# Kernel optimization log

Measured on AMD Instinct MI355X. Metric: run time of the kernel, lower is better.

The kernel has to match this reference:

```python
import jax, jax.numpy as jnp
import numpy as np

N, E, D, H, LAYERS = 50000, 800000, 128, 8, 2
LRELU_ALPHA = 0.2


def _seg_softmax(logits, seg, n):
    # numerically stable softmax over edges grouped by destination node
    m = jax.ops.segment_max(logits, seg, num_segments=n)
    z = jnp.exp(logits - m[seg])
    s = jax.ops.segment_sum(z, seg, num_segments=n)
    return z / jnp.maximum(s[seg], 1e-16)


def _gat_layer(x, src, dst, W, a_src, a_dst, concat):
    # W: [H, Fin, F'], a_src/a_dst: [H, F']
    n = x.shape[0]
    outs = []
    for h in range(W.shape[0]):  # loop over heads to bound peak memory
        Wh = x @ W[h]                              # [N, F']
        es = Wh @ a_src[h]                         # [N]
        ed = Wh @ a_dst[h]                         # [N]
        e = jax.nn.leaky_relu(es[src] + ed[dst], LRELU_ALPHA)  # [E]
        att = _seg_softmax(e, dst, n)              # [E]
        out = jax.ops.segment_sum(att[:, None] * Wh[src], dst, num_segments=n)
        outs.append(out)
    if concat:
        return jax.nn.elu(jnp.concatenate(outs, axis=-1))  # [N, H*F']
    return jnp.mean(jnp.stack(outs, axis=0), axis=0)        # [N, F']


def _rel_gcn_layer(x, src, dst, w, W):
    # weighted-adjacency GCN with row (in-degree) normalization + ReLU
    n = x.shape[0]
    deg = jax.ops.segment_sum(w, dst, num_segments=n)
    norm = w / jnp.maximum(deg[dst], 1e-16)        # [E]
    h = x @ W                                      # [N, Dout]
    agg = jax.ops.segment_sum(norm[:, None] * h[src], dst, num_segments=n)
    return jax.nn.relu(agg)


def setup_inputs() -> dict:
    key = jax.random.key(0)
    ks = jax.random.split(key, 12)
    s = 1.0 / np.sqrt(D)
    return {
        "x": jax.random.normal(ks[0], (N, D), dtype=jnp.float32),
        "edge_index": jax.random.randint(ks[1], (2, E), 0, N, dtype=jnp.int64),
        "edge_weight": jax.random.uniform(ks[2], (E,), dtype=jnp.float32),
        "gat_W0": jax.random.normal(ks[3], (H, D, D // H), dtype=jnp.float32) * s,
        "gat_a0_src": jax.random.normal(ks[4], (H, D // H), dtype=jnp.float32) * s,
        "gat_a0_dst": jax.random.normal(ks[5], (H, D // H), dtype=jnp.float32) * s,
        "gat_W1": jax.random.normal(ks[6], (H, D, D), dtype=jnp.float32) * s,
        "gat_a1_src": jax.random.normal(ks[7], (H, D), dtype=jnp.float32) * s,
        "gat_a1_dst": jax.random.normal(ks[8], (H, D), dtype=jnp.float32) * s,
        "gcn_W0": jax.random.normal(ks[9], (D, D), dtype=jnp.float32) * s,
        "gcn_W1": jax.random.normal(ks[10], (D, D), dtype=jnp.float32) * s,
    }


def reference(x, edge_index, edge_weight, gat_W0, gat_a0_src, gat_a0_dst,
              gat_W1, gat_a1_src, gat_a1_dst, gcn_W0, gcn_W1):
    src, dst = edge_index[0], edge_index[1]
    gat_params = [(gat_W0, gat_a0_src, gat_a0_dst), (gat_W1, gat_a1_src, gat_a1_dst)]
    gcn_params = [gcn_W0, gcn_W1]
    x1, x2 = x, x  # dropout is identity in eval mode
    for i in range(LAYERS):
        W, a_s, a_d = gat_params[i]
        x1 = _gat_layer(x1, src, dst, W, a_s, a_d, concat=(i != LAYERS - 1))
        x2 = _rel_gcn_layer(x2, src, dst, edge_weight, gcn_params[i])
    # cat along new last dim then MaxPool1d(2) == elementwise max of branches
    return jnp.maximum(x1, x2)
```

## Files before the change

### kernel.cpp

```cpp
#include <hip/hip_runtime.h>

#define LRELU_ALPHA 0.2f

typedef __attribute__((ext_vector_type(8))) short short8;
typedef __attribute__((ext_vector_type(4))) float float4v;
typedef __attribute__((ext_vector_type(2))) float f32x2;

__device__ __forceinline__ unsigned short f2bf(float f) {
  union { float f; unsigned u; } x; x.f = f;
  unsigned r = (x.u + 0x7fff + ((x.u >> 16) & 1)) >> 16;
  return (unsigned short)r;
}
__device__ __forceinline__ float bflo(unsigned u) {
  union { unsigned u; float f; } x; x.u = u << 16; return x.f;
}
__device__ __forceinline__ float bfhi(unsigned u) {
  union { unsigned u; float f; } x; x.u = u & 0xffff0000u; return x.f;
}
__device__ __forceinline__ f32x2 bfpair(unsigned u) {
  return (f32x2){bflo(u), bfhi(u)};
}
__device__ __forceinline__ unsigned packbf(float a, float b) {
  return (unsigned)f2bf(a) | ((unsigned)f2bf(b) << 16);
}


__global__ __launch_bounds__(256) void k_count(const int* __restrict__ dst,
                                               int* __restrict__ cnt, int E) {
  int e = blockIdx.x * 256 + threadIdx.x;
  if (e < E) atomicAdd(&cnt[dst[e]], 1);
}

__global__ __launch_bounds__(1024) void k_scan1(const int* __restrict__ cnt,
                                                int* __restrict__ lscan,
                                                int* __restrict__ bsum, int N) {
  __shared__ int sm[1024];
  int t = threadIdx.x;
  int base = blockIdx.x * 1024;
  int v = (base + t < N) ? cnt[base + t] : 0;
  sm[t] = v;
  __syncthreads();
  for (int off = 1; off < 1024; off <<= 1) {
    int x = (t >= off) ? sm[t - off] : 0;
    __syncthreads();
    sm[t] += x;
    __syncthreads();
  }
  if (base + t < N) lscan[base + t] = sm[t] - v;
  if (t == 1023) bsum[blockIdx.x] = sm[1023];
}

__global__ __launch_bounds__(64) void k_scan2(int* __restrict__ bsum,
                                              int* __restrict__ rowptrN, int nb) {
  int t = threadIdx.x;
  int v = (t < nb) ? bsum[t] : 0;
  int orig = v;
  for (int off = 1; off < 64; off <<= 1) {
    int y = __shfl_up(v, off, 64);
    if (t >= off) v += y;
  }
  if (t < nb) bsum[t] = v - orig;
  if (t == 63) *rowptrN = v;
}

__global__ __launch_bounds__(1024) void k_scan3(int* __restrict__ rowptr,
                                                int* __restrict__ cur,
                                                const int* __restrict__ bsum, int N) {
  int i = blockIdx.x * 1024 + threadIdx.x;
  if (i < N) {
    int v = rowptr[i] + bsum[blockIdx.x];
    rowptr[i] = v;
    cur[i] = v;
  }
}

__global__ __launch_bounds__(256) void k_scatter(const int* __restrict__ src,
                                                 const int* __restrict__ dst,
                                                 const float* __restrict__ w,
                                                 const float* __restrict__ logit0,
                                                 int* __restrict__ cur,
                                                 uint2* __restrict__ edata,
                                                 unsigned short* __restrict__ pedge,
                                                 int E) {
  int base = (blockIdx.x * 256 + threadIdx.x) * 4;
  if (base >= E) return;
  int n = E - base; if (n > 4) n = 4;
  int ss[4], dd[4]; float ww[4];
  if (n == 4) {
    int4 s4 = *(const int4*)(src + base);
    int4 d4 = *(const int4*)(dst + base);
    float4 w4 = *(const float4*)(w + base);
    ss[0] = s4.x; ss[1] = s4.y; ss[2] = s4.z; ss[3] = s4.w;
    dd[0] = d4.x; dd[1] = d4.y; dd[2] = d4.z; dd[3] = d4.w;
    ww[0] = w4.x; ww[1] = w4.y; ww[2] = w4.z; ww[3] = w4.w;
  } else {
    for (int i = 0; i < n; ++i) { ss[i] = src[base + i]; dd[i] = dst[base + i]; ww[i] = w[base + i]; }
  }
  int pp[4];
#pragma unroll
  for (int i = 0; i < 4; ++i)
    if (i < n) pp[i] = atomicAdd(&cur[dd[i]], 1);
#pragma unroll
  for (int i = 0; i < 4; ++i) {
    if (i >= n) break;
    int s = ss[i], d = dd[i], p = pp[i];
    edata[p] = make_uint2((unsigned)s, __float_as_uint(ww[i]));
    float4 es0 = *(const float4*)(logit0 + (size_t)s * 16);
    float4 es1 = *(const float4*)(logit0 + (size_t)s * 16 + 4);
    float4 ed0 = *(const float4*)(logit0 + (size_t)d * 16 + 8);
    float4 ed1 = *(const float4*)(logit0 + (size_t)d * 16 + 12);
    float lg[8] = {es0.x + ed0.x, es0.y + ed0.y, es0.z + ed0.z, es0.w + ed0.w,
                   es1.x + ed1.x, es1.y + ed1.y, es1.z + ed1.z, es1.w + ed1.w};
    unsigned short o[8];
#pragma unroll
    for (int h = 0; h < 8; ++h) {
      float v = lg[h] > 0.f ? lg[h] : LRELU_ALPHA * lg[h];
      o[h] = f2bf(__expf(fminf(v, 80.f)));
    }
    ushort4 q0 = {o[0], o[1], o[2], o[3]};
    ushort4 q1 = {o[4], o[5], o[6], o[7]};
    *(ushort4*)(pedge + (size_t)p * 8) = q0;
    *(ushort4*)(pedge + (size_t)p * 8 + 4) = q1;
  }
}

__global__ __launch_bounds__(256) void k_pack(const float* __restrict__ W0,
                                              const float* __restrict__ a0s,
                                              const float* __restrict__ a0d,
                                              const float* __restrict__ W1,
                                              const float* __restrict__ a1s,
                                              const float* __restrict__ a1d,
                                              const float* __restrict__ gw0,
                                              const float* __restrict__ gw1,
                                              unsigned short* __restrict__ W0catT,
                                              float* __restrict__ logitW,
                                              unsigned short* __restrict__ gw1T,
                                              unsigned short* __restrict__ va1T,
                                              unsigned short* __restrict__ WstackT) {
  int idx = blockIdx.x * 256 + threadIdx.x;
  if (idx < 32768) {
    int n = idx >> 7, k = idx & 127;
    float v;
    if (n < 128) {
      int h = n >> 4, f = n & 15;
      v = W0[h * 2048 + k * 16 + f];
    } else {
      v = gw0[k * 128 + (n - 128)];
    }
    W0catT[idx] = f2bf(v);
  } else if (idx < 34816) {
    int j = idx - 32768;
    int k = j >> 4, c = j & 15;
    int h = (c < 8) ? c : c - 8;
    const float* a = (c < 8) ? a0s : a0d;
    float s = 0.f;
    for (int f = 0; f < 16; ++f) s += W0[h * 2048 + k * 16 + f] * a[h * 16 + f];
    logitW[j] = s;
  } else if (idx < 51200) {
    int j = idx - 34816;
    int n = j >> 7, k = j & 127;
    gw1T[j] = f2bf(gw1[k * 128 + n]);
  } else if (idx < 53248) {
    int j = idx - 51200;
    int c = j >> 7, k = j & 127;
    int h = c & 7;
    const float* a = (c < 8) ? a1s : a1d;
    float s = 0.f;
    for (int f = 0; f < 128; ++f) s += W1[h * 16384 + k * 128 + f] * a[h * 128 + f];
    va1T[j] = f2bf(s);
  } else if (idx < 184320) {
    int j = idx - 53248;
    int n = j >> 10, kk = j & 1023;
    int h = kk >> 7, k = kk & 127;
    WstackT[j] = f2bf(W1[h * 16384 + k * 128 + n] * 0.125f);
  }
}

__global__ __launch_bounds__(256) void k_prep(const float* __restrict__ x,
                                              const float* __restrict__ logitW,
                                              unsigned short* __restrict__ xb,
                                              float* __restrict__ logit0, int N) {
  __shared__ float sm[16][132];
  __shared__ float sw[2048];
  int t = threadIdx.x;
  int base = blockIdx.x * 16;
  int r = t >> 4, cc = (t & 15) * 8;
  const float* xr = x + (size_t)(base + r) * 128 + cc;
  float4 v0 = *(const float4*)xr;
  float4 v1 = *(const float4*)(xr + 4);
  ushort4 o0 = {f2bf(v0.x), f2bf(v0.y), f2bf(v0.z), f2bf(v0.w)};
  ushort4 o1 = {f2bf(v1.x), f2bf(v1.y), f2bf(v1.z), f2bf(v1.w)};
  *(ushort4*)(xb + (size_t)(base + r) * 128 + cc) = o0;
  *(ushort4*)(xb + (size_t)(base + r) * 128 + cc + 4) = o1;
  *(float4*)&sm[r][cc] = v0;
  *(float4*)&sm[r][cc + 4] = v1;
  *(float4*)&sw[t * 8] = *(const float4*)(logitW + t * 8);
  *(float4*)&sw[t * 8 + 4] = *(const float4*)(logitW + t * 8 + 4);
  __syncthreads();
  int c = t & 15;
  float acc = 0.f;
#pragma unroll
  for (int k = 0; k < 128; ++k) acc += sm[r][k] * sw[k * 16 + c];
  logit0[(size_t)(base + r) * 16 + c] = acc;
}

__global__ __launch_bounds__(256) void k_pedge(const float* __restrict__ logits,
                                               const uint2* __restrict__ edata,
                                               const int* __restrict__ rowptr,
                                               unsigned short* __restrict__ pedge,
                                               float* __restrict__ linv, int N) {
  int wave = threadIdx.x >> 6, lane = threadIdx.x & 63;
  int d = blockIdx.x * 4 + wave;
  if (d >= N) return;
  int j8 = lane >> 3, h = lane & 7;
  float edv = logits[(size_t)d * 16 + 8 + h];
  int beg = rowptr[d], end = rowptr[d + 1];
  float lsum = 0.f;
  for (int ii = beg + j8; ii < end; ii += 8) {
    unsigned s = edata[ii].x;
    float es = logits[(size_t)s * 16 + h];
    float lg = es + edv;
    lg = lg > 0.f ? lg : LRELU_ALPHA * lg;
    float p = __expf(fminf(lg, 80.f));
    lsum += p;
    pedge[(size_t)ii * 8 + h] = f2bf(p);
  }
  lsum += __shfl_xor(lsum, 8, 64);
  lsum += __shfl_xor(lsum, 16, 64);
  lsum += __shfl_xor(lsum, 32, 64);
  if (lane < 8) linv[(size_t)d * 8 + h] = lsum > 0.f ? 1.f / lsum : 0.f;
}

template <int NT, int OUT_BF16, int EPI>
__global__ __launch_bounds__(256) void k_mgemm(const unsigned short* __restrict__ A, int lda,
                                               const unsigned short* __restrict__ BT, int ldb,
                                               void* __restrict__ Cv, int ldc,
                                               const void* __restrict__ aux,
                                               int M, int Ncols, int K) {
  __shared__ unsigned short As[64][64];
  __shared__ unsigned short Bs[NT * 16][64];
  int tid = threadIdx.x;
  int w = tid >> 6, lane = tid & 63;
  int quad = lane >> 4, l16 = lane & 15;
  int row0 = blockIdx.x * 64;
  int c0 = blockIdx.y * (NT * 16);
  float4v acc[NT];
#pragma unroll
  for (int t = 0; t < NT; ++t) acc[t] = (float4v){0.f, 0.f, 0.f, 0.f};

  for (int k0 = 0; k0 < K; k0 += 64) {
    __syncthreads();
#pragma unroll
    for (int i = 0; i < 2; ++i) {
      int c = tid + i * 256;
      int r = c >> 3, kc = c & 7;
      uint4 v = {0u, 0u, 0u, 0u};
      int gr = row0 + r;
      if (gr < M) v = *(const uint4*)(A + (size_t)gr * lda + k0 + kc * 8);
      *(uint4*)(&As[r][(kc ^ (r & 7)) * 8]) = v;
    }
#pragma unroll
    for (int i = 0; i < (NT * 128 + 255) / 256; ++i) {
      int c = tid + i * 256;
      if (c < NT * 128) {
        int n = c >> 3, kc = c & 7;
        uint4 v = {0u, 0u, 0u, 0u};
        int gn = c0 + n;
        if (gn < Ncols) v = *(const uint4*)(BT + (size_t)gn * ldb + k0 + kc * 8);
        *(uint4*)(&Bs[n][(kc ^ (n & 7)) * 8]) = v;
      }
    }
    __syncthreads();
#pragma unroll
    for (int ks = 0; ks < 2; ++ks) {
      int m = w * 16 + l16;
      int ga = (ks * 4 + quad) ^ (m & 7);
      short8 a = *(const short8*)(&As[m][ga * 8]);
#pragma unroll
      for (int t = 0; t < NT; ++t) {
        int n = t * 16 + l16;
        int gb = (ks * 4 + quad) ^ (n & 7);
        short8 b = *(const short8*)(&Bs[n][gb * 8]);
        acc[t] = __builtin_amdgcn_mfma_f32_16x16x32_bf16(a, b, acc[t], 0, 0, 0);
      }
    }
  }
#pragma unroll
  for (int t = 0; t < NT; ++t) {
    int cc = c0 + t * 16 + l16;
    if (cc >= Ncols) continue;
#pragma unroll
    for (int i = 0; i < 4; ++i) {
      int rr = row0 + w * 16 + quad * 4 + i;
      if (rr >= M) continue;
      float v = acc[t][i];
      if (EPI == 1) {
        unsigned short us = ((const unsigned short*)aux)[(size_t)rr * ldc + cc];
        v = fmaxf(v, bflo((unsigned)us));
      }
      if (EPI == 2) {
        ((unsigned short*)Cv)[(size_t)rr * 256 + 4 * (cc >> 1) + 2 + (cc & 1)] = f2bf(v);
      } else if (EPI == 4) {
        if (cc < 128) {
          ((unsigned short*)Cv)[(size_t)rr * 128 + cc] = f2bf(v);
        } else {
          int enc = __builtin_amdgcn_cvt_pk_fp8_f32(v, v, 0, false);
          ((unsigned char*)aux)[(size_t)rr * 128 + (cc - 128)] = (unsigned char)(enc & 0xff);
        }
      } else if (OUT_BF16)
        ((unsigned short*)Cv)[(size_t)rr * ldc + cc] = f2bf(v);
      else
        ((float*)Cv)[(size_t)rr * ldc + cc] = v;
    }
  }
}

__global__ __launch_bounds__(256) void k_agg0(const unsigned short* __restrict__ featg,
                                              const unsigned char* __restrict__ featc,
                                              const int* __restrict__ rowptr,
                                              const uint2* __restrict__ edata,
                                              const unsigned short* __restrict__ pedge,
                                              unsigned short* __restrict__ x1c,
                                              unsigned short* __restrict__ x2,
                                              unsigned short* __restrict__ xh, int N) {
  __shared__ uint2 swl[4][64];
  __shared__ float pl[4][512];
  int wave = threadIdx.x >> 6, lane = threadIdx.x & 63;
  int d = blockIdx.x * 4 + wave;
  if (d >= N) return;
  int half = lane >> 5, lane2 = lane & 31;
  int head = lane2 >> 2;
  int beg = rowptr[d], end = rowptr[d + 1], deg = end - beg;
  f32x2 aa = {0.f, 0.f}, ab = {0.f, 0.f}, ga = {0.f, 0.f}, gb = {0.f, 0.f};
  float l = 0.f, wsum = 0.f;
  for (int base = 0; base < deg; base += 64) {
    int idx = beg + base + lane;
    uint2 sv = make_uint2(0u, 0u);
    uint4 q = make_uint4(0u, 0u, 0u, 0u);
    if (idx < end) {
      sv = edata[idx];
      q = *(const uint4*)(pedge + (size_t)idx * 8);
    }
    swl[wave][lane] = sv;
    float4 pa = make_float4(bflo(q.x), bfhi(q.x), bflo(q.y), bfhi(q.y));
    float4 pb = make_float4(bflo(q.z), bfhi(q.z), bflo(q.w), bfhi(q.w));
    *(float4*)&pl[wave][lane * 8] = pa;
    *(float4*)&pl[wave][lane * 8 + 4] = pb;
    int ng = deg - base; if (ng > 64) ng = 64;
    int tp = (ng + 1) >> 1;
    int t = 0;
    for (; t + 2 <= tp; t += 2) {
      int e0 = 2 * t + half, e1 = e0 + 2;
      uint2 sw0 = swl[wave][e0], sw1 = swl[wave][e1];
      float p0 = pl[wave][e0 * 8 + head], p1 = pl[wave][e1 * 8 + head];
      uint2 g0 = ((const uint2*)featg)[(size_t)sw0.x * 32 + lane2];
      unsigned c0v = ((const unsigned*)featc)[(size_t)sw0.x * 32 + lane2];
      uint2 g1 = ((const uint2*)featg)[(size_t)sw1.x * 32 + lane2];
      unsigned c1v = ((const unsigned*)featc)[(size_t)sw1.x * 32 + lane2];
      float w0 = __uint_as_float(sw0.y), w1 = __uint_as_float(sw1.y);
      aa += bfpair(g0.x) * p0;
      ab += bfpair(g0.y) * p0;
      ga += __builtin_amdgcn_cvt_pk_f32_fp8(c0v, false) * w0;
      gb += __builtin_amdgcn_cvt_pk_f32_fp8(c0v, true) * w0;
      l += p0; wsum += w0;
      aa += bfpair(g1.x) * p1;
      ab += bfpair(g1.y) * p1;
      ga += __builtin_amdgcn_cvt_pk_f32_fp8(c1v, false) * w1;
      gb += __builtin_amdgcn_cvt_pk_f32_fp8(c1v, true) * w1;
      l += p1; wsum += w1;
    }
    for (; t < tp; ++t) {
      int e = 2 * t + half;
      uint2 sw = swl[wave][e];
      float p = pl[wave][e * 8 + head];
      float wj = __uint_as_float(sw.y);
      uint2 g = ((const uint2*)featg)[(size_t)sw.x * 32 + lane2];
      unsigned cv = ((const unsigned*)featc)[(size_t)sw.x * 32 + lane2];
      aa += bfpair(g.x) * p;
      ab += bfpair(g.y) * p;
      ga += __builtin_amdgcn_cvt_pk_f32_fp8(cv, false) * wj;
      gb += __builtin_amdgcn_cvt_pk_f32_fp8(cv, true) * wj;
      l += p; wsum += wj;
    }
  }
  aa.x += __shfl_xor(aa.x, 32, 64); aa.y += __shfl_xor(aa.y, 32, 64);
  ab.x += __shfl_xor(ab.x, 32, 64); ab.y += __shfl_xor(ab.y, 32, 64);
  ga.x += __shfl_xor(ga.x, 32, 64); ga.y += __shfl_xor(ga.y, 32, 64);
  gb.x += __shfl_xor(gb.x, 32, 64); gb.y += __shfl_xor(gb.y, 32, 64);
  l += __shfl_xor(l, 32, 64);
  wsum += __shfl_xor(wsum, 32, 64);
  if (half == 0) {
    float inv = l > 0.f ? 1.f / l : 0.f;
    float v0 = aa.x * inv, v1 = aa.y * inv, v2 = ab.x * inv, v3 = ab.y * inv;
    v0 = v0 > 0.f ? v0 : __expf(v0) - 1.f;
    v1 = v1 > 0.f ? v1 : __expf(v1) - 1.f;
    v2 = v2 > 0.f ? v2 : __expf(v2) - 1.f;
    v3 = v3 > 0.f ? v3 : __expf(v3) - 1.f;
    unsigned p0 = packbf(v0, v1), p1 = packbf(v2, v3);
    ((uint2*)x1c)[(size_t)d * 32 + lane2] = make_uint2(p0, p1);
    ((unsigned*)xh)[(size_t)d * 128 + 4 * lane2] = p0;
    ((unsigned*)xh)[(size_t)d * 128 + 4 * lane2 + 2] = p1;
    float ginv = 1.f / fmaxf(wsum, 1e-16f);
    float w0 = fmaxf(ga.x * ginv, 0.f), w1 = fmaxf(ga.y * ginv, 0.f);
    float w2 = fmaxf(gb.x * ginv, 0.f), w3 = fmaxf(gb.y * ginv, 0.f);
    ((uint2*)x2)[(size_t)d * 32 + lane2] = make_uint2(packbf(w0, w1), packbf(w2, w3));
  }
}

__global__ __launch_bounds__(256) void k_agg1(const unsigned short* __restrict__ xh,
                                              const int* __restrict__ rowptr,
                                              const uint2* __restrict__ edata,
                                              const unsigned short* __restrict__ pedge,
                                              const float* __restrict__ linv,
                                              unsigned short* __restrict__ aggbuf,
                                              unsigned short* __restrict__ x2f, int N) {
  __shared__ uint2 swl[4][64];
  __shared__ float pl[4][512];
  int wave = threadIdx.x >> 6, lane = threadIdx.x & 63;
  int d = blockIdx.x * 4 + wave;
  if (d >= N) return;
  int half = lane >> 5, lane2 = lane & 31;
  int beg = rowptr[d], end = rowptr[d + 1], deg = end - beg;
  f32x2 axA[8] = {}, axB[8] = {};
  f32x2 ga = {0.f, 0.f}, gb = {0.f, 0.f};
  float wsum = 0.f;
  for (int base = 0; base < deg; base += 64) {
    int idx = beg + base + lane;
    uint2 sv = make_uint2(0u, 0u);
    uint4 q = make_uint4(0u, 0u, 0u, 0u);
    if (idx < end) {
      sv = edata[idx];
      q = *(const uint4*)(pedge + (size_t)idx * 8);
    }
    swl[wave][lane] = sv;
    float4 pa = make_float4(bflo(q.x), bfhi(q.x), bflo(q.y), bfhi(q.y));
    float4 pb = make_float4(bflo(q.z), bfhi(q.z), bflo(q.w), bfhi(q.w));
    *(float4*)&pl[wave][lane * 8] = pa;
    *(float4*)&pl[wave][lane * 8 + 4] = pb;
    int ng = deg - base; if (ng > 64) ng = 64;
    int tp = (ng + 1) >> 1;
    for (int t = 0; t < tp; ++t) {
      int e = 2 * t + half;
      uint2 sw = swl[wave][e];
      float4 pv0 = *(const float4*)&pl[wave][e * 8];
      float4 pv1 = *(const float4*)&pl[wave][e * 8 + 4];
      float wj = __uint_as_float(sw.y);
      uint4 u = *(const uint4*)(xh + (size_t)sw.x * 256 + 8 * lane2);
      f32x2 xA = bfpair(u.x), hA = bfpair(u.y);
      f32x2 xB = bfpair(u.z), hB = bfpair(u.w);
      ga += hA * wj;
      gb += hB * wj;
      wsum += wj;
      axA[0] += xA * pv0.x; axB[0] += xB * pv0.x;
      axA[1] += xA * pv0.y; axB[1] += xB * pv0.y;
      axA[2] += xA * pv0.z; axB[2] += xB * pv0.z;
      axA[3] += xA * pv0.w; axB[3] += xB * pv0.w;
      axA[4] += xA * pv1.x; axB[4] += xB * pv1.x;
      axA[5] += xA * pv1.y; axB[5] += xB * pv1.y;
      axA[6] += xA * pv1.z; axB[6] += xB * pv1.z;
      axA[7] += xA * pv1.w; axB[7] += xB * pv1.w;
    }
  }
#pragma unroll
  for (int h = 0; h < 8; ++h) {
    axA[h].x += __shfl_xor(axA[h].x, 32, 64); axA[h].y += __shfl_xor(axA[h].y, 32, 64);
    axB[h].x += __shfl_xor(axB[h].x, 32, 64); axB[h].y += __shfl_xor(axB[h].y, 32, 64);
  }
  ga.x += __shfl_xor(ga.x, 32, 64); ga.y += __shfl_xor(ga.y, 32, 64);
  gb.x += __shfl_xor(gb.x, 32, 64); gb.y += __shfl_xor(gb.y, 32, 64);
  wsum += __shfl_xor(wsum, 32, 64);
  if (half == 0) {
    float4 i0 = *(const float4*)(linv + (size_t)d * 8);
    float4 i1 = *(const float4*)(linv + (size_t)d * 8 + 4);
    float invh[8] = {i0.x, i0.y, i0.z, i0.w, i1.x, i1.y, i1.z, i1.w};
    size_t lr2 = (size_t)d * 256;
#pragma unroll
    for (int h = 0; h < 8; ++h) {
      ((uint2*)aggbuf)[lr2 + h * 32 + lane2] =
          make_uint2(packbf(axA[h].x * invh[h], axA[h].y * invh[h]),
                     packbf(axB[h].x * invh[h], axB[h].y * invh[h]));
    }
    float ginv = 1.f / fmaxf(wsum, 1e-16f);
    float w0 = fmaxf(ga.x * ginv, 0.f), w1 = fmaxf(ga.y * ginv, 0.f);
    float w2 = fmaxf(gb.x * ginv, 0.f), w3 = fmaxf(gb.y * ginv, 0.f);
    ((uint2*)x2f)[(size_t)d * 32 + lane2] = make_uint2(packbf(w0, w1), packbf(w2, w3));
  }
}


extern "C" void kernel_launch(void* const* d_in, const int* in_sizes, int n_in,
                              void* d_out, int out_size, void* d_ws, size_t ws_size,
                              hipStream_t stream) {
  const float* x   = (const float*)d_in[0];
  const int*   ei  = (const int*)d_in[1];
  const float* ew  = (const float*)d_in[2];
  const float* W0  = (const float*)d_in[3];
  const float* a0s = (const float*)d_in[4];
  const float* a0d = (const float*)d_in[5];
  const float* W1  = (const float*)d_in[6];
  const float* a1s = (const float*)d_in[7];
  const float* a1d = (const float*)d_in[8];
  const float* gw0 = (const float*)d_in[9];
  const float* gw1 = (const float*)d_in[10];
  float* out = (float*)d_out;

  const int N = in_sizes[0] / 128;
  const int E = in_sizes[1] / 2;
  const int* src = ei;
  const int* dst = ei + E;

  char* p = (char*)d_ws;
  auto carve = [&](size_t bytes) {
    void* r = (void*)p;
    p += (bytes + 255) & ~(size_t)255;
    return r;
  };
  int*   cnt    = (int*)carve((size_t)N * 4);
  int*   rowptr = (int*)carve((size_t)(N + 1) * 4);
  int*   cur    = (int*)carve((size_t)N * 4);
  int*   bsum   = (int*)carve(256 * 4);
  uint2* edata  = (uint2*)carve((size_t)E * 8);
  unsigned short* W0catT  = (unsigned short*)carve(32768 * 2);
  float*          logitW  = (float*)carve(2048 * 4);
  unsigned short* gw1T    = (unsigned short*)carve(16384 * 2);
  unsigned short* va1T    = (unsigned short*)carve(2048 * 2);
  unsigned short* WstackT = (unsigned short*)carve(131072 * 2);
  unsigned short* x2   = (unsigned short*)carve((size_t)N * 128 * 2);
  float*          esed = (float*)carve((size_t)N * 16 * 4);
  unsigned short* xh   = (unsigned short*)carve((size_t)N * 256 * 2);
  unsigned short* pedge = (unsigned short*)carve((size_t)E * 8 * 2);
  float*          linv1 = (float*)carve((size_t)N * 8 * 4);
  size_t ph1 = ((size_t)N * 128 * 2 + 255) & ~(size_t)255;
  size_t ph2 = ph1 + (((size_t)N * 128 * 2 + 255) & ~(size_t)255);
  size_t ph3 = ph2 + (((size_t)N * 128 + 255) & ~(size_t)255);
  size_t ph4 = ph3 + (((size_t)N * 16 * 4 + 255) & ~(size_t)255);
  size_t scratch_sz = (size_t)N * 1024 * 2;
  if (ph4 > scratch_sz) scratch_sz = ph4;
  char* scratch = (char*)carve(scratch_sz);
  unsigned short* xb     = (unsigned short*)scratch;
  unsigned short* x1c    = (unsigned short*)scratch;
  unsigned short* featg  = (unsigned short*)(scratch + ph1);
  unsigned char*  featc  = (unsigned char*)(scratch + ph2);
  float*          logit0 = (float*)(scratch + ph3);
  unsigned short* aggbuf = (unsigned short*)scratch;
  unsigned short* x2f    = x2;

  int gE = (E + 255) / 256;
  int gE4 = ((E + 3) / 4 + 255) / 256;
  int nb = (N + 1023) / 1024;
  int gM = (N + 63) / 64;
  int gD = (N + 3) / 4;

  hipMemsetAsync(cnt, 0, (size_t)N * 4, stream);
  k_count<<<gE, 256, 0, stream>>>(dst, cnt, E);
  k_scan1<<<nb, 1024, 0, stream>>>(cnt, rowptr, bsum, N);
  k_scan2<<<1, 64, 0, stream>>>(bsum, rowptr + N, nb);
  k_scan3<<<nb, 1024, 0, stream>>>(rowptr, cur, bsum, N);

  k_pack<<<(184320 + 255) / 256, 256, 0, stream>>>(W0, a0s, a0d, W1, a1s, a1d, gw0,
                                                   gw1, W0catT, logitW, gw1T, va1T,
                                                   WstackT);
  k_prep<<<(N + 15) / 16, 256, 0, stream>>>(x, logitW, xb, logit0, N);

  k_scatter<<<gE4, 256, 0, stream>>>(src, dst, ew, logit0, cur, edata, pedge, E);

  k_mgemm<8, 1, 4><<<dim3(gM, 2), 256, 0, stream>>>(xb, 128, W0catT, 128, featg, 128,
                                                    featc, N, 256, 128);
  k_agg0<<<gD, 256, 0, stream>>>(featg, featc, rowptr, edata, pedge, x1c, x2, xh, N);

  k_mgemm<1, 0, 0><<<dim3(gM, 1), 256, 0, stream>>>(x1c, 128, va1T, 128, esed, 16,
                                                    nullptr, N, 16, 128);
  k_mgemm<8, 1, 2><<<dim3(gM, 1), 256, 0, stream>>>(x2, 128, gw1T, 128, xh, 256,
                                                    nullptr, N, 128, 128);

  k_pedge<<<gD, 256, 0, stream>>>(esed, edata, rowptr, pedge, linv1, N);

  k_agg1<<<gD, 256, 0, stream>>>(xh, rowptr, edata, pedge, linv1, aggbuf, x2f, N);

  k_mgemm<8, 0, 1><<<dim3(gM, 1), 256, 0, stream>>>(aggbuf, 1024, WstackT, 1024, out,
                                                    128, x2f, N, 128, 1024);
}
```

Measured before the change: 448.4 us.

## Use full-wave per-edge gathers and persistent grid-stride loops in aggregation kernels

The two edge-aggregation kernels now use all 64 lanes of a wave on one edge's feature row with narrower per-lane loads, instead of splitting the wave into two halves that handle alternate edges and then combining them with cross-lane shuffles. Each wave processes edges in groups of four to keep more independent gathers in flight. The grid is capped at 2048 blocks and each wave loops over destination nodes, with launch bounds raised to request 8 blocks per CU. This removes the shuffle reduction and halves per-lane register accumulators, but each load is narrower and low-degree nodes may leave fewer loads outstanding per wave.

Measured after the change: 458.6 us. 2.3% more time.

```diff
diff --git a/kernel.cpp b/kernel.cpp
--- a/kernel.cpp
+++ b/kernel.cpp
@@ -315,175 +315,164 @@
   }
 }
 
-__global__ __launch_bounds__(256) void k_agg0(const unsigned short* __restrict__ featg,
-                                              const unsigned char* __restrict__ featc,
-                                              const int* __restrict__ rowptr,
-                                              const uint2* __restrict__ edata,
-                                              const unsigned short* __restrict__ pedge,
-                                              unsigned short* __restrict__ x1c,
-                                              unsigned short* __restrict__ x2,
-                                              unsigned short* __restrict__ xh, int N) {
+__global__ __launch_bounds__(256, 8) void k_agg0(const unsigned short* __restrict__ featg,
+                                                 const unsigned char* __restrict__ featc,
+                                                 const int* __restrict__ rowptr,
+                                                 const uint2* __restrict__ edata,
+                                                 const unsigned short* __restrict__ pedge,
+                                                 unsigned short* __restrict__ x1c,
+                                                 unsigned short* __restrict__ x2,
+                                                 unsigned short* __restrict__ xh, int N) {
   __shared__ uint2 swl[4][64];
   __shared__ float pl[4][512];
   int wave = threadIdx.x >> 6, lane = threadIdx.x & 63;
-  int d = blockIdx.x * 4 + wave;
-  if (d >= N) return;
-  int half = lane >> 5, lane2 = lane & 31;
-  int head = lane2 >> 2;
-  int beg = rowptr[d], end = rowptr[d + 1], deg = end - beg;
-  f32x2 aa = {0.f, 0.f}, ab = {0.f, 0.f}, ga = {0.f, 0.f}, gb = {0.f, 0.f};
-  float l = 0.f, wsum = 0.f;
-  for (int base = 0; base < deg; base += 64) {
-    int idx = beg + base + lane;
-    uint2 sv = make_uint2(0u, 0u);
-    uint4 q = make_uint4(0u, 0u, 0u, 0u);
-    if (idx < end) {
-      sv = edata[idx];
-      q = *(const uint4*)(pedge + (size_t)idx * 8);
-    }
-    swl[wave][lane] = sv;
-    float4 pa = make_float4(bflo(q.x), bfhi(q.x), bflo(q.y), bfhi(q.y));
-    float4 pb = make_float4(bflo(q.z), bfhi(q.z), bflo(q.w), bfhi(q.w));
-    *(float4*)&pl[wave][lane * 8] = pa;
-    *(float4*)&pl[wave][lane * 8 + 4] = pb;
-    int ng = deg - base; if (ng > 64) ng = 64;
-    int tp = (ng + 1) >> 1;
-    int t = 0;
-    for (; t + 2 <= tp; t += 2) {
-      int e0 = 2 * t + half, e1 = e0 + 2;
-      uint2 sw0 = swl[wave][e0], sw1 = swl[wave][e1];
-      float p0 = pl[wave][e0 * 8 + head], p1 = pl[wave][e1 * 8 + head];
-      uint2 g0 = ((const uint2*)featg)[(size_t)sw0.x * 32 + lane2];
-      unsigned c0v = ((const unsigned*)featc)[(size_t)sw0.x * 32 + lane2];
-      uint2 g1 = ((const uint2*)featg)[(size_t)sw1.x * 32 + lane2];
-      unsigned c1v = ((const unsigned*)featc)[(size_t)sw1.x * 32 + lane2];
-      float w0 = __uint_as_float(sw0.y), w1 = __uint_as_float(sw1.y);
-      aa += bfpair(g0.x) * p0;
-      ab += bfpair(g0.y) * p0;
-      ga += __builtin_amdgcn_cvt_pk_f32_fp8(c0v, false) * w0;
-      gb += __builtin_amdgcn_cvt_pk_f32_fp8(c0v, true) * w0;
-      l += p0; wsum += w0;
-      aa += bfpair(g1.x) * p1;
-      ab += bfpair(g1.y) * p1;
-      ga += __builtin_amdgcn_cvt_pk_f32_fp8(c1v, false) * w1;
-      gb += __builtin_amdgcn_cvt_pk_f32_fp8(c1v, true) * w1;
-      l += p1; wsum += w1;
-    }
-    for (; t < tp; ++t) {
-      int e = 2 * t + half;
-      uint2 sw = swl[wave][e];
-      float p = pl[wave][e * 8 + head];
-      float wj = __uint_as_float(sw.y);
-      uint2 g = ((const uint2*)featg)[(size_t)sw.x * 32 + lane2];
-      unsigned cv = ((const unsigned*)featc)[(size_t)sw.x * 32 + lane2];
-      aa += bfpair(g.x) * p;
-      ab += bfpair(g.y) * p;
-      ga += __builtin_amdgcn_cvt_pk_f32_fp8(cv, false) * wj;
-      gb += __builtin_amdgcn_cvt_pk_f32_fp8(cv, true) * wj;
-      l += p; wsum += wj;
-    }
-  }
-  aa.x += __shfl_xor(aa.x, 32, 64); aa.y += __shfl_xor(aa.y, 32, 64);
-  ab.x += __shfl_xor(ab.x, 32, 64); ab.y += __shfl_xor(ab.y, 32, 64);
-  ga.x += __shfl_xor(ga.x, 32, 64); ga.y += __shfl_xor(ga.y, 32, 64);
-  gb.x += __shfl_xor(gb.x, 32, 64); gb.y += __shfl_xor(gb.y, 32, 64);
-  l += __shfl_xor(l, 32, 64);
-  wsum += __shfl_xor(wsum, 32, 64);
-  if (half == 0) {
+  int head = lane >> 3;
+  const unsigned* FG = (const unsigned*)featg + lane;
+  const unsigned short* FC = (const unsigned short*)featc + lane;
+  for (int d = blockIdx.x * 4 + wave; d < N; d += gridDim.x * 4) {
+    int beg = rowptr[d], end = rowptr[d + 1], deg = end - beg;
+    f32x2 aa = {0.f, 0.f}, ga = {0.f, 0.f};
+    float l = 0.f, wsum = 0.f;
+    for (int base = 0; base < deg; base += 64) {
+      int idx = beg + base + lane;
+      uint2 sv = make_uint2(0u, 0u);
+      uint4 q = make_uint4(0u, 0u, 0u, 0u);
+      if (idx < end) {
+        sv = edata[idx];
+        q = *(const uint4*)(pedge + (size_t)idx * 8);
+      }
+      swl[wave][lane] = sv;
+      float4 pa = make_float4(bflo(q.x), bfhi(q.x), bflo(q.y), bfhi(q.y));
+      float4 pb = make_float4(bflo(q.z), bfhi(q.z), bflo(q.w), bfhi(q.w));
+      *(float4*)&pl[wave][lane * 8] = pa;
+      *(float4*)&pl[wave][lane * 8 + 4] = pb;
+      int ng = deg - base; if (ng > 64) ng = 64;
+      int t = 0;
+      for (; t + 4 <= ng; t += 4) {
+        uint2 s0 = swl[wave][t], s1 = swl[wave][t + 1];
+        uint2 s2 = swl[wave][t + 2], s3 = swl[wave][t + 3];
+        unsigned g0 = FG[(size_t)s0.x * 64];
+        unsigned g1 = FG[(size_t)s1.x * 64];
+        unsigned g2 = FG[(size_t)s2.x * 64];
+        unsigned g3 = FG[(size_t)s3.x * 64];
+        unsigned c0 = (unsigned)FC[(size_t)s0.x * 64];
+        unsigned c1 = (unsigned)FC[(size_t)s1.x * 64];
+        unsigned c2 = (unsigned)FC[(size_t)s2.x * 64];
+        unsigned c3 = (unsigned)FC[(size_t)s3.x * 64];
+        float p0 = pl[wave][t * 8 + head];
+        float p1 = pl[wave][t * 8 + 8 + head];
+        float p2 = pl[wave][t * 8 + 16 + head];
+        float p3 = pl[wave][t * 8 + 24 + head];
+        float w0 = __uint_as_float(s0.y), w1 = __uint_as_float(s1.y);
+        float w2 = __uint_as_float(s2.y), w3 = __uint_as_float(s3.y);
+        aa += bfpair(g0) * p0; ga += __builtin_amdgcn_cvt_pk_f32_fp8(c0, false) * w0;
+        l += p0; wsum += w0;
+        aa += bfpair(g1) * p1; ga += __builtin_amdgcn_cvt_pk_f32_fp8(c1, false) * w1;
+        l += p1; wsum += w1;
+        aa += bfpair(g2) * p2; ga += __builtin_amdgcn_cvt_pk_f32_fp8(c2, false) * w2;
+        l += p2; wsum += w2;
+        aa += bfpair(g3) * p3; ga += __builtin_amdgcn_cvt_pk_f32_fp8(c3, false) * w3;
+        l += p3; wsum += w3;
+      }
+      for (; t < ng; ++t) {
+        uint2 s0 = swl[wave][t];
+        unsigned g0 = FG[(size_t)s0.x * 64];
+        unsigned c0 = (unsigned)FC[(size_t)s0.x * 64];
+        float p0 = pl[wave][t * 8 + head];
+        float w0 = __uint_as_float(s0.y);
+        aa += bfpair(g0) * p0; ga += __builtin_amdgcn_cvt_pk_f32_fp8(c0, false) * w0;
+        l += p0; wsum += w0;
+      }
+    }
     float inv = l > 0.f ? 1.f / l : 0.f;
-    float v0 = aa.x * inv, v1 = aa.y * inv, v2 = ab.x * inv, v3 = ab.y * inv;
+    float v0 = aa.x * inv, v1 = aa.y * inv;
     v0 = v0 > 0.f ? v0 : __expf(v0) - 1.f;
     v1 = v1 > 0.f ? v1 : __expf(v1) - 1.f;
-    v2 = v2 > 0.f ? v2 : __expf(v2) - 1.f;
-    v3 = v3 > 0.f ? v3 : __expf(v3) - 1.f;
-    unsigned p0 = packbf(v0, v1), p1 = packbf(v2, v3);
-    ((uint2*)x1c)[(size_t)d * 32 + lane2] = make_uint2(p0, p1);
-    ((unsigned*)xh)[(size_t)d * 128 + 4 * lane2] = p0;
-    ((unsigned*)xh)[(size_t)d * 128 + 4 * lane2 + 2] = p1;
+    unsigned p0 = packbf(v0, v1);
+    ((unsigned*)x1c)[(size_t)d * 64 + lane] = p0;
+    ((unsigned*)xh)[(size_t)d * 128 + 2 * lane] = p0;
     float ginv = 1.f / fmaxf(wsum, 1e-16f);
-    float w0 = fmaxf(ga.x * ginv, 0.f), w1 = fmaxf(ga.y * ginv, 0.f);
-    float w2 = fmaxf(gb.x * ginv, 0.f), w3 = fmaxf(gb.y * ginv, 0.f);
-    ((uint2*)x2)[(size_t)d * 32 + lane2] = make_uint2(packbf(w0, w1), packbf(w2, w3));
-  }
-}
-
-__global__ __launch_bounds__(256) void k_agg1(const unsigned short* __restrict__ xh,
-                                              const int* __restrict__ rowptr,
-                                              const uint2* __restrict__ edata,
-                                              const unsigned short* __restrict__ pedge,
-                                              const float* __restrict__ linv,
-                                              unsigned short* __restrict__ aggbuf,
-                                              unsigned short* __restrict__ x2f, int N) {
+    ((unsigned*)x2)[(size_t)d * 64 + lane] =
+        packbf(fmaxf(ga.x * ginv, 0.f), fmaxf(ga.y * ginv, 0.f));
+  }
+}
+
+__global__ __launch_bounds__(256, 8) void k_agg1(const unsigned short* __restrict__ xh,
+                                                 const int* __restrict__ rowptr,
+                                                 const uint2* __restrict__ edata,
+                                                 const unsigned short* __restrict__ pedge,
+                                                 const float* __restrict__ linv,
+                                                 unsigned short* __restrict__ aggbuf,
+                                                 unsigned short* __restrict__ x2f, int N) {
   __shared__ uint2 swl[4][64];
   __shared__ float pl[4][512];
   int wave = threadIdx.x >> 6, lane = threadIdx.x & 63;
-  int d = blockIdx.x * 4 + wave;
-  if (d >= N) return;
-  int half = lane >> 5, lane2 = lane & 31;
-  int beg = rowptr[d], end = rowptr[d + 1], deg = end - beg;
-  f32x2 axA[8] = {}, axB[8] = {};
-  f32x2 ga = {0.f, 0.f}, gb = {0.f, 0.f};
-  float wsum = 0.f;
-  for (int base = 0; base < deg; base += 64) {
-    int idx = beg + base + lane;
-    uint2 sv = make_uint2(0u, 0u);
-    uint4 q = make_uint4(0u, 0u, 0u, 0u);
-    if (idx < end) {
-      sv = edata[idx];
-      q = *(const uint4*)(pedge + (size_t)idx * 8);
-    }
-    swl[wave][lane] = sv;
-    float4 pa = make_float4(bflo(q.x), bfhi(q.x), bflo(q.y), bfhi(q.y));
-    float4 pb = make_float4(bflo(q.z), bfhi(q.z), bflo(q.w), bfhi(q.w));
-    *(float4*)&pl[wave][lane * 8] = pa;
-    *(float4*)&pl[wave][lane * 8 + 4] = pb;
-    int ng = deg - base; if (ng > 64) ng = 64;
-    int tp = (ng + 1) >> 1;
-    for (int t = 0; t < tp; ++t) {
-      int e = 2 * t + half;
-      uint2 sw = swl[wave][e];
-      float4 pv0 = *(const float4*)&pl[wave][e * 8];
-      float4 pv1 = *(const float4*)&pl[wave][e * 8 + 4];
-      float wj = __uint_as_float(sw.y);
-      uint4 u = *(const uint4*)(xh + (size_t)sw.x * 256 + 8 * lane2);
-      f32x2 xA = bfpair(u.x), hA = bfpair(u.y);
-      f32x2 xB = bfpair(u.z), hB = bfpair(u.w);
-      ga += hA * wj;
-      gb += hB * wj;
-      wsum += wj;
-      axA[0] += xA * pv0.x; axB[0] += xB * pv0.x;
-      axA[1] += xA * pv0.y; axB[1] += xB * pv0.y;
-      axA[2] += xA * pv0.z; axB[2] += xB * pv0.z;
-      axA[3] += xA * pv0.w; axB[3] += xB * pv0.w;
-      axA[4] += xA * pv1.x; axB[4] += xB * pv1.x;
-      axA[5] += xA * pv1.y; axB[5] += xB * pv1.y;
-      axA[6] += xA * pv1.z; axB[6] += xB * pv1.z;
-      axA[7] += xA * pv1.w; axB[7] += xB * pv1.w;
-    }
-  }
-#pragma unroll
-  for (int h = 0; h < 8; ++h) {
-    axA[h].x += __shfl_xor(axA[h].x, 32, 64); axA[h].y += __shfl_xor(axA[h].y, 32, 64);
-    axB[h].x += __shfl_xor(axB[h].x, 32, 64); axB[h].y += __shfl_xor(axB[h].y, 32, 64);
-  }
-  ga.x += __shfl_xor(ga.x, 32, 64); ga.y += __shfl_xor(ga.y, 32, 64);
-  gb.x += __shfl_xor(gb.x, 32, 64); gb.y += __shfl_xor(gb.y, 32, 64);
-  wsum += __shfl_xor(wsum, 32, 64);
-  if (half == 0) {
+  const uint2* X2 = (const uint2*)xh + lane;
+  for (int d = blockIdx.x * 4 + wave; d < N; d += gridDim.x * 4) {
+    int beg = rowptr[d], end = rowptr[d + 1], deg = end - beg;
+    f32x2 axp[8] = {};
+    f32x2 gp = {0.f, 0.f};
+    float wsum = 0.f;
+#define EDGE1(uu, ss, tt)                                    \
+  {                                                          \
+    float4 pv0 = *(const float4*)&pl[wave][(tt) * 8];        \
+    float4 pv1 = *(const float4*)&pl[wave][(tt) * 8 + 4];    \
+    float wj = __uint_as_float((ss).y);                      \
+    f32x2 xA = bfpair((uu).x), hA = bfpair((uu).y);          \
+    axp[0] += xA * pv0.x; axp[1] += xA * pv0.y;              \
+    axp[2] += xA * pv0.z; axp[3] += xA * pv0.w;              \
+    axp[4] += xA * pv1.x; axp[5] += xA * pv1.y;              \
+    axp[6] += xA * pv1.z; axp[7] += xA * pv1.w;              \
+    gp += hA * wj; wsum += wj;                               \
+  }
+    for (int base = 0; base < deg; base += 64) {
+      int idx = beg + base + lane;
+      uint2 sv = make_uint2(0u, 0u);
+      uint4 q = make_uint4(0u, 0u, 0u, 0u);
+      if (idx < end) {
+        sv = edata[idx];
+        q = *(const uint4*)(pedge + (size_t)idx * 8);
+      }
+      swl[wave][lane] = sv;
+      float4 pa = make_float4(bflo(q.x), bfhi(q.x), bflo(q.y), bfhi(q.y));
+      float4 pb = make_float4(bflo(q.z), bfhi(q.z), bflo(q.w), bfhi(q.w));
+      *(float4*)&pl[wave][lane * 8] = pa;
+      *(float4*)&pl[wave][lane * 8 + 4] = pb;
+      int ng = deg - base; if (ng > 64) ng = 64;
+      int t = 0;
+      for (; t + 4 <= ng; t += 4) {
+        uint2 s0 = swl[wave][t], s1 = swl[wave][t + 1];
+        uint2 s2 = swl[wave][t + 2], s3 = swl[wave][t + 3];
+        uint2 u0 = X2[(size_t)s0.x * 64];
+        uint2 u1 = X2[(size_t)s1.x * 64];
+        uint2 u2 = X2[(size_t)s2.x * 64];
+        uint2 u3 = X2[(size_t)s3.x * 64];
+        EDGE1(u0, s0, t)
+        EDGE1(u1, s1, t + 1)
+        EDGE1(u2, s2, t + 2)
+        EDGE1(u3, s3, t + 3)
+      }
+      for (; t < ng; ++t) {
+        uint2 s0 = swl[wave][t];
+        uint2 u0 = X2[(size_t)s0.x * 64];
+        EDGE1(u0, s0, t)
+      }
+    }
+#undef EDGE1
     float4 i0 = *(const float4*)(linv + (size_t)d * 8);
     float4 i1 = *(const float4*)(linv + (size_t)d * 8 + 4);
-    float invh[8] = {i0.x, i0.y, i0.z, i0.w, i1.x, i1.y, i1.z, i1.w};
-    size_t lr2 = (size_t)d * 256;
-#pragma unroll
-    for (int h = 0; h < 8; ++h) {
-      ((uint2*)aggbuf)[lr2 + h * 32 + lane2] =
-          make_uint2(packbf(axA[h].x * invh[h], axA[h].y * invh[h]),
-                     packbf(axB[h].x * invh[h], axB[h].y * invh[h]));
-    }
+    unsigned* ab = (unsigned*)aggbuf + (size_t)d * 512 + lane;
+    ab[0]   = packbf(axp[0].x * i0.x, axp[0].y * i0.x);
+    ab[64]  = packbf(axp[1].x * i0.y, axp[1].y * i0.y);
+    ab[128] = packbf(axp[2].x * i0.z, axp[2].y * i0.z);
+    ab[192] = packbf(axp[3].x * i0.w, axp[3].y * i0.w);
+    ab[256] = packbf(axp[4].x * i1.x, axp[4].y * i1.x);
+    ab[320] = packbf(axp[5].x * i1.y, axp[5].y * i1.y);
+    ab[384] = packbf(axp[6].x * i1.z, axp[6].y * i1.z);
+    ab[448] = packbf(axp[7].x * i1.w, axp[7].y * i1.w);
     float ginv = 1.f / fmaxf(wsum, 1e-16f);
-    float w0 = fmaxf(ga.x * ginv, 0.f), w1 = fmaxf(ga.y * ginv, 0.f);
-    float w2 = fmaxf(gb.x * ginv, 0.f), w3 = fmaxf(gb.y * ginv, 0.f);
-    ((uint2*)x2f)[(size_t)d * 32 + lane2] = make_uint2(packbf(w0, w1), packbf(w2, w3));
+    ((unsigned*)x2f)[(size_t)d * 64 + lane] =
+        packbf(fmaxf(gp.x * ginv, 0.f), fmaxf(gp.y * ginv, 0.f));
   }
 }
 
@@ -550,6 +539,7 @@
   int nb = (N + 1023) / 1024;
   int gM = (N + 63) / 64;
   int gD = (N + 3) / 4;
+  int gA = gD < 2048 ? gD : 2048;
 
   hipMemsetAsync(cnt, 0, (size_t)N * 4, stream);
   k_count<<<gE, 256, 0, stream>>>(dst, cnt, E);
@@ -566,7 +556,7 @@
 
   k_mgemm<8, 1, 4><<<dim3(gM, 2), 256, 0, stream>>>(xb, 128, W0catT, 128, featg, 128,
                                                     featc, N, 256, 128);
-  k_agg0<<<gD, 256, 0, stream>>>(featg, featc, rowptr, edata, pedge, x1c, x2, xh, N);
+  k_agg0<<<gA, 256, 0, stream>>>(featg, featc, rowptr, edata, pedge, x1c, x2, xh, N);
 
   k_mgemm<1, 0, 0><<<dim3(gM, 1), 256, 0, stream>>>(x1c, 128, va1T, 128, esed, 16,
                                                     nullptr, N, 16, 128);
@@ -575,7 +565,7 @@
 
   k_pedge<<<gD, 256, 0, stream>>>(esed, edata, rowptr, pedge, linv1, N);
 
-  k_agg1<<<gD, 256, 0, stream>>>(xh, rowptr, edata, pedge, linv1, aggbuf, x2f, N);
+  k_agg1<<<gA, 256, 0, stream>>>(xh, rowptr, edata, pedge, linv1, aggbuf, x2f, N);
 
   k_mgemm<8, 0, 1><<<dim3(gM, 1), 256, 0, stream>>>(aggbuf, 1024, WstackT, 1024, out,
                                                     128, x2f, N, 128, 1024);
```
